# Kernel tuning notes

Measured on AMD Instinct MI355X. Metric: run time of the kernel, lower is better.

The kernel has to match this reference:

```python
import jax, jax.numpy as jnp
import numpy as np

N_ATOMS = 5000
N_EDGES = 100000
F = 128          # num_features
B = 20           # num_basis (sinc expansion)
L = 3            # num_interactions
CUTOFF = 5.0
NUM_EMB = 119


def setup_inputs() -> dict:
    key = jax.random.key(0)
    ks = jax.random.split(key, 16)
    Z = jax.random.randint(ks[0], (N_ATOMS,), 1, NUM_EMB)
    edge_idx = jax.random.randint(ks[1], (N_EDGES, 2), 0, N_ATOMS)
    edge_dist = jax.random.uniform(ks[2], (N_EDGES,), minval=0.5, maxval=6.0, dtype=jnp.float32)
    u = jax.random.normal(ks[3], (N_EDGES, 3), dtype=jnp.float32)
    u = u / jnp.linalg.norm(u, axis=-1, keepdims=True)
    edge_diff = u * edge_dist[:, None]  # displacement vectors with |d| == edge_dist
    s = lambda k, shape: (jax.random.normal(k, shape, dtype=jnp.float32) * 0.05)
    inp = dict(Z=Z, edge_idx=edge_idx, edge_diff=edge_diff, edge_dist=edge_dist)
    inp.update(
        emb=s(ks[4], (NUM_EMB, F)),
        msg_w1=s(ks[5], (L, F, F)), msg_b1=jnp.zeros((L, F), jnp.float32),
        msg_w2=s(ks[6], (L, F, 3 * F)), msg_b2=jnp.zeros((L, 3 * F), jnp.float32),
        filt_w=s(ks[7], (L, B, 3 * F)), filt_b=jnp.zeros((L, 3 * F), jnp.float32),
        upd_U=s(ks[8], (L, F, F)), upd_V=s(ks[9], (L, F, F)),
        upd_w1=s(ks[10], (L, 2 * F, F)), upd_b1=jnp.zeros((L, F), jnp.float32),
        upd_w2=s(ks[11], (L, F, 3 * F)), upd_b2=jnp.zeros((L, 3 * F), jnp.float32),
        ro_w1=s(ks[12], (F, F // 2)), ro_b1=jnp.zeros((F // 2,), jnp.float32),
        ro_w2=s(ks[13], (F // 2, 1)), ro_b2=jnp.zeros((1,), jnp.float32),
    )
    return inp


def _painn(Z, edge_idx, edge_diff, edge_dist,
           emb, msg_w1, msg_b1, msg_w2, msg_b2, filt_w, filt_b,
           upd_U, upd_V, upd_w1, upd_b1, upd_w2, upd_b2,
           ro_w1, ro_b1, ro_w2, ro_b2):
    dtype = edge_diff.dtype
    # edge mask (equivalent to boolean compaction: masked edges contribute 0)
    mask = (edge_dist < CUTOFF).astype(dtype)
    dst = edge_idx[:, 0]  # receiver (index_add target)
    src = edge_idx[:, 1]  # sender (gathered neighbor)
    # sinc radial expansion: sin(n*pi*r/rc)/r, n = 1..B
    n = jnp.arange(1, B + 1, dtype=dtype)
    rbf = jnp.sin(edge_dist[:, None] * n * (jnp.pi / CUTOFF)) / edge_dist[:, None]  # [E,B]
    # cosine cutoff envelope, zeroed outside cutoff
    fc = 0.5 * (jnp.cos(jnp.pi * edge_dist / CUTOFF) + 1.0)
    env = (fc * mask)[:, None]  # [E,1]
    unit = edge_diff / edge_dist[:, None]  # [E,3]

    s_feat = emb[Z]                                   # [N,F]
    v_feat = jnp.zeros((Z.shape[0], 3, F), dtype)     # [N,3,F]

    for l in range(L):
        # ---- PainnMessage ----
        filt = (rbf @ filt_w[l] + filt_b[l]) * env                           # [E,3F]
        phi = jax.nn.silu(s_feat @ msg_w1[l] + msg_b1[l]) @ msg_w2[l] + msg_b2[l]  # [N,3F]
        fo = filt * phi[src]                                                  # [E,3F]
        gsv, gev, ms = jnp.split(fo, 3, axis=-1)                              # each [E,F]
        mv = v_feat[src] * gsv[:, None, :] + gev[:, None, :] * unit[:, :, None]  # [E,3,F]
        s_feat = s_feat + jnp.zeros_like(s_feat).at[dst].add(ms)
        v_feat = v_feat + jnp.zeros_like(v_feat).at[dst].add(mv)
        # ---- PainnUpdate ----
        Uv = jnp.einsum('nif,fg->nig', v_feat, upd_U[l])   # [N,3,F]
        Vv = jnp.einsum('nif,fg->nig', v_feat, upd_V[l])   # [N,3,F]
        Vn = jnp.linalg.norm(Vv, axis=1)                   # [N,F]
        a = jax.nn.silu(jnp.concatenate([s_feat, Vn], axis=-1) @ upd_w1[l] + upd_b1[l]) @ upd_w2[l] + upd_b2[l]
        avv, asv, ass = jnp.split(a, 3, axis=-1)
        v_feat = v_feat + avv[:, None, :] * Uv
        s_feat = s_feat + asv * jnp.sum(Uv * Vv, axis=1) + ass

    # atomwise readout MLP -> per-atom energy
    atom_energy = (jax.nn.silu(s_feat @ ro_w1 + ro_b1) @ ro_w2 + ro_b2)[:, 0]  # [N]
    return atom_energy


def reference(Z, edge_idx, edge_diff, edge_dist,
              emb, msg_w1, msg_b1, msg_w2, msg_b2, filt_w, filt_b,
              upd_U, upd_V, upd_w1, upd_b1, upd_w2, upd_b2,
              ro_w1, ro_b1, ro_w2, ro_b2):
    return _painn(Z, edge_idx, edge_diff, edge_dist,
                  emb, msg_w1, msg_b1, msg_w2, msg_b2, filt_w, filt_b,
                  upd_U, upd_V, upd_w1, upd_b1, upd_w2, upd_b2,
                  ro_w1, ro_b1, ro_w2, ro_b2)
```

## Files before the change

kernel.cpp:

```cpp
#include <hip/hip_runtime.h>
#include <hip/hip_bf16.h>
#include <hip/hip_fp16.h>
#include <math.h>

#define N_ATOMS 5000
#define N_EDGES 100000
#define F 128
#define B 20
#define NL 3
#define CAP 64

constexpr float CUTOFF = 5.0f;
constexpr float PI_F = 3.14159265358979323846f;

typedef _Float16 f16x8 __attribute__((ext_vector_type(8)));
typedef _Float16 h2 __attribute__((ext_vector_type(2)));
typedef float f32x4 __attribute__((ext_vector_type(4)));

struct EMeta { int src; float env; float u0, u1, u2; int pad[3]; };

__device__ __forceinline__ float silu_f(float x) { return x / (1.0f + __expf(-x)); }

#define PV_IDX(atom, t) (((size_t)(atom) * F + (t)) * 8)

__global__ void init_kernel(const int* __restrict__ Z, const float* __restrict__ emb,
                            float* __restrict__ s, _Float16* __restrict__ s_h,
                            float* __restrict__ v, _Float16* __restrict__ pv,
                            int* __restrict__ count) {
    int atom = blockIdx.x;
    int t = threadIdx.x;
    float val = emb[Z[atom] * F + t];
    s[atom * F + t] = val;
    s_h[atom * F + t] = (_Float16)val;
#pragma unroll
    for (int d = 0; d < 3; ++d) v[(size_t)atom * 3 * F + d * F + t] = 0.0f;
    f16x8 z = {};
    *(f16x8*)(pv + PV_IDX(atom, t)) = z;
    if (t == 0) count[atom] = 0;
}

__global__ void fill_buckets(const int* __restrict__ eidx, int* __restrict__ count,
                             int* __restrict__ bucket) {
    int e = blockIdx.x * 256 + threadIdx.x;
    if (e >= N_EDGES) return;
    int dst = eidx[2 * e];
    int pos = atomicAdd(&count[dst], 1);
    if (pos < CAP) bucket[dst * CAP + pos] = e;
}

__global__ void edge_meta_kernel(const int* __restrict__ count, const int* __restrict__ bucket,
                                 const int* __restrict__ eidx, const float* __restrict__ ediff,
                                 const float* __restrict__ edist,
                                 EMeta* __restrict__ meta, _Float16* __restrict__ rbfh) {
    int slot = blockIdx.x * 256 + threadIdx.x;
    if (slot >= N_ATOMS * CAP) return;
    int a = slot / CAP, i = slot % CAP;
    if (i >= count[a]) return;
    int e = bucket[slot];
    float d = edist[e];
    EMeta m;
    m.src = eidx[2 * e + 1];
    float fc = 0.5f * (cosf(PI_F * d / CUTOFF) + 1.0f);
    m.env = (d < CUTOFF) ? fc : 0.0f;
    float inv = 1.0f / d;
    m.u0 = ediff[3 * e + 0] * inv;
    m.u1 = ediff[3 * e + 1] * inv;
    m.u2 = ediff[3 * e + 2] * inv;
    m.pad[0] = m.pad[1] = m.pad[2] = 0;
    meta[slot] = m;
    _Float16* rp = rbfh + (size_t)slot * 24;
#pragma unroll
    for (int b = 0; b < B; ++b)
        rp[b] = (_Float16)(sinf(d * (float)(b + 1) * (PI_F / CUTOFF)) / d);
    rp[20] = rp[21] = rp[22] = rp[23] = (_Float16)0.0f;
}

struct TPlanX { const float* src; void* dst; int R, C, blk0, isf16, pad; };
struct TPlansX { TPlanX p[24]; int n; };

__global__ void transpose_x(TPlansX P) {
    int b = blockIdx.x;
    int pi = 0;
#pragma unroll
    for (int i = 1; i < 24; ++i)
        if (i < P.n && b >= P.p[i].blk0) pi = i;
    const float* src = P.p[pi].src;
    int R = P.p[pi].R, C = P.p[pi].C, pad = P.p[pi].pad;
    int f = (b - P.p[pi].blk0) * 256 + threadIdx.x;
    if (f < R * C) {
        int c = f / R, r = f - c * R;
        float val = src[r * C + c];
        if (P.p[pi].isf16) ((_Float16*)P.p[pi].dst)[c * pad + r] = (_Float16)val;
        else ((float*)P.p[pi].dst)[c * pad + r] = val;
    }
}

__global__ __launch_bounds__(256) void phi_mlp_kernel(
    const _Float16* __restrict__ s_h, const _Float16* __restrict__ w1T,
    const float* __restrict__ b1, const _Float16* __restrict__ w2T,
    const float* __restrict__ b2, _Float16* __restrict__ pv) {
    __shared__ __align__(16) _Float16 shA[16 * 136];
    __shared__ __align__(16) _Float16 shH[16 * 136];
    int r0 = blockIdx.x * 16;
    int tid = threadIdx.x;
    {
        int r = tid >> 4, c8 = (tid & 15) * 8;
        int rg = r0 + r; if (rg >= N_ATOMS) rg = N_ATOMS - 1;
        *(f16x8*)(shA + r * 136 + c8) = *(const f16x8*)(s_h + (size_t)rg * F + c8);
    }
    __syncthreads();
    int lane = tid & 63, wv = tid >> 6;
    int col = lane & 15, quad = lane >> 4;
    for (int nt = wv; nt < 8; nt += 4) {
        int n = nt * 16 + col;
        f32x4 acc = {0.f, 0.f, 0.f, 0.f};
#pragma unroll
        for (int kt = 0; kt < 4; ++kt) {
            f16x8 afr = *(const f16x8*)(shA + col * 136 + kt * 32 + quad * 8);
            f16x8 bfr = *(const f16x8*)(w1T + (size_t)n * 128 + kt * 32 + quad * 8);
            acc = __builtin_amdgcn_mfma_f32_16x16x32_f16(afr, bfr, acc, 0, 0, 0);
        }
        float bb = b1[n];
#pragma unroll
        for (int r = 0; r < 4; ++r)
            shH[(quad * 4 + r) * 136 + n] = (_Float16)silu_f(acc[r] + bb);
    }
    __syncthreads();
    for (int nt = wv; nt < 24; nt += 4) {
        int n = nt * 16 + col;
        f32x4 acc = {0.f, 0.f, 0.f, 0.f};
#pragma unroll
        for (int kt = 0; kt < 4; ++kt) {
            f16x8 afr = *(const f16x8*)(shH + col * 136 + kt * 32 + quad * 8);
            f16x8 bfr = *(const f16x8*)(w2T + (size_t)n * 128 + kt * 32 + quad * 8);
            acc = __builtin_amdgcn_mfma_f32_16x16x32_f16(afr, bfr, acc, 0, 0, 0);
        }
        float bb = b2[n];
#pragma unroll
        for (int r = 0; r < 4; ++r) {
            int row = r0 + quad * 4 + r;
            if (row < N_ATOMS)
                pv[PV_IDX(row, n & 127) + (n >> 7)] = (_Float16)(acc[r] + bb);
        }
    }
}

__global__ __launch_bounds__(256) void edge_agg_kernel(
    const int* __restrict__ count, const EMeta* __restrict__ meta,
    const _Float16* __restrict__ rbfh,
    const _Float16* __restrict__ fwT,
    const float* __restrict__ fb,
    const _Float16* __restrict__ pv,
    float* __restrict__ s, float* __restrict__ v,
    _Float16* __restrict__ vmid_h) {
    int a = blockIdx.x;
    int tid = threadIdx.x;
    int t = tid & 127;
    int team = tid >> 7;

    unsigned int rw0[10], rw1[10], rw2[10];
    {
        const unsigned int* p0 = (const unsigned int*)(fwT + (size_t)t * 24);
        const unsigned int* p1 = (const unsigned int*)(fwT + (size_t)(F + t) * 24);
        const unsigned int* p2 = (const unsigned int*)(fwT + (size_t)(2 * F + t) * 24);
#pragma unroll
        for (int j = 0; j < 10; ++j) { rw0[j] = p0[j]; rw1[j] = p1[j]; rw2[j] = p2[j]; }
    }
    float fb0 = fb[t], fb1 = fb[F + t], fb2 = fb[2 * F + t];

    int n = count[a]; if (n > CAP) n = CAP;
    float accS = 0.f, accV0 = 0.f, accV1 = 0.f, accV2 = 0.f;

    __shared__ int sh_src[32];
    __shared__ float sh_env[32];
    __shared__ float sh_unit[32][3];
    __shared__ __align__(16) unsigned int sh_rbf[32 * 12];
    __shared__ __align__(16) float sh_part[4][F];
    const size_t aC = (size_t)a * CAP;
    const unsigned int* rbf32 = (const unsigned int*)rbfh;

    for (int base = 0; base < n; base += 32) {
        int cnt = min(32, n - base);
        __syncthreads();
        if (tid < cnt) {
            EMeta m = meta[aC + base + tid];
            sh_src[tid] = m.src;
            sh_env[tid] = m.env;
            sh_unit[tid][0] = m.u0; sh_unit[tid][1] = m.u1; sh_unit[tid][2] = m.u2;
        }
        for (int task = tid; task < cnt * 12; task += 256) {
            int i = task / 12, w = task - i * 12;
            sh_rbf[i * 12 + w] = rbf32[(aC + base + i) * 12 + w];
        }
        __syncthreads();

        int myCnt = (cnt > team) ? ((cnt - team + 1) >> 1) : 0;
        if (myCnt > 0) {
            f16x8 QA[4], QB[4];
            int ngrp = (myCnt + 3) >> 2;

            auto load_grp = [&](int gbase, f16x8 Q[4]) {
#pragma unroll
                for (int j = 0; j < 4; ++j) {
                    int i = gbase + j;
                    int ii = (i < myCnt) ? i : (myCnt - 1);
                    int src = sh_src[team + 2 * ii];
                    Q[j] = *(const f16x8*)(pv + PV_IDX(src, t));
                }
            };
            auto comp_grp = [&](int gbase, f16x8 Q[4]) {
#pragma unroll
                for (int j = 0; j < 4; ++j) {
                    int i = gbase + j;
                    if (i < myCnt) {
                        int ei = team + 2 * i;
                        const uint4* rq = (const uint4*)(sh_rbf + ei * 12);
                        uint4 qa = rq[0], qb = rq[1];
                        uint2 qc = *(const uint2*)(sh_rbf + ei * 12 + 8);
                        unsigned int rr[10] = {qa.x, qa.y, qa.z, qa.w,
                                               qb.x, qb.y, qb.z, qb.w, qc.x, qc.y};
                        float f0 = fb0, f1 = fb1, f2 = fb2;
#pragma unroll
                        for (int p = 0; p < 10; ++p) {
                            h2 rb = __builtin_bit_cast(h2, rr[p]);
                            f0 = __builtin_amdgcn_fdot2(rb, __builtin_bit_cast(h2, rw0[p]), f0, false);
                            f1 = __builtin_amdgcn_fdot2(rb, __builtin_bit_cast(h2, rw1[p]), f1, false);
                            f2 = __builtin_amdgcn_fdot2(rb, __builtin_bit_cast(h2, rw2[p]), f2, false);
                        }
                        float env = sh_env[ei];
                        f0 *= env; f1 *= env; f2 *= env;
                        accS += f2 * (float)Q[j][2];
                        float gsv = f0 * (float)Q[j][0];
                        float gev = f1 * (float)Q[j][1];
                        accV0 += (float)Q[j][3] * gsv + gev * sh_unit[ei][0];
                        accV1 += (float)Q[j][4] * gsv + gev * sh_unit[ei][1];
                        accV2 += (float)Q[j][5] * gsv + gev * sh_unit[ei][2];
                    }
                }
            };

            load_grp(0, QA);
            for (int g = 0; g < ngrp; g += 2) {
                if (g + 1 < ngrp) load_grp((g + 1) * 4, QB);
                comp_grp(g * 4, QA);
                if (g + 1 < ngrp) {
                    if (g + 2 < ngrp) load_grp((g + 2) * 4, QA);
                    comp_grp((g + 1) * 4, QB);
                }
            }
        }
    }

    __syncthreads();
    if (team == 1) {
        sh_part[0][t] = accS; sh_part[1][t] = accV0;
        sh_part[2][t] = accV1; sh_part[3][t] = accV2;
    }
    __syncthreads();
    if (team == 0) {
        float sm = s[a * F + t] + accS + sh_part[0][t];
        s[a * F + t] = sm;
        float vm0 = v[a * 3 * F + t] + accV0 + sh_part[1][t];
        float vm1 = v[a * 3 * F + F + t] + accV1 + sh_part[2][t];
        float vm2 = v[a * 3 * F + 2 * F + t] + accV2 + sh_part[3][t];
        v[a * 3 * F + t] = vm0;
        v[a * 3 * F + F + t] = vm1;
        v[a * 3 * F + 2 * F + t] = vm2;
        vmid_h[(size_t)(a * 3 + 0) * F + t] = (_Float16)vm0;
        vmid_h[(size_t)(a * 3 + 1) * F + t] = (_Float16)vm1;
        vmid_h[(size_t)(a * 3 + 2) * F + t] = (_Float16)vm2;
    }
}

__global__ __launch_bounds__(512) void fused_update_kernel(
    const _Float16* __restrict__ vmid_h, const _Float16* __restrict__ uvT,
    const _Float16* __restrict__ w1T, const float* __restrict__ b1,
    const _Float16* __restrict__ w2T, const float* __restrict__ b2,
    float* __restrict__ s, float* __restrict__ v, _Float16* __restrict__ pv,
    const _Float16* __restrict__ nw1T, const float* __restrict__ nb1,
    const _Float16* __restrict__ nw2T, const float* __restrict__ nb2,
    int do_phi,
    const _Float16* __restrict__ roT16, const float* __restrict__ rb1,
    const float* __restrict__ rw2, const float* __restrict__ rb2,
    float* __restrict__ out, int do_ro) {
    __shared__ __align__(16) _Float16 shA[48 * 136];
    __shared__ __align__(16) _Float16 shUV[48 * 264];
    __shared__ __align__(16) _Float16 shCat[16 * 264];
    __shared__ __align__(16) _Float16 shH[16 * 136];
    __shared__ __align__(16) _Float16 shAa[16 * 392];
    _Float16* shS = shA;
    float* shRO = (float*)shAa;
    int a0 = blockIdx.x * 16;
    int r0 = a0 * 3;
    int tid = threadIdx.x;
    for (int slot = tid; slot < 48 * 16; slot += 512) {
        int r = slot >> 4, c8 = (slot & 15) * 8;
        int rg = r0 + r; if (rg >= N_ATOMS * 3) rg = N_ATOMS * 3 - 1;
        *(f16x8*)(shA + r * 136 + c8) = *(const f16x8*)(vmid_h + (size_t)rg * F + c8);
    }
    __syncthreads();
    int lane = tid & 63, wv = tid >> 6;
    int col = lane & 15, quad = lane >> 4;

    for (int j = wv; j < 48; j += 8) {
        int mt = j >> 4, nt = j & 15;
        int n = nt * 16 + col;
        f32x4 acc = {0.f, 0.f, 0.f, 0.f};
#pragma unroll
        for (int kt = 0; kt < 4; ++kt) {
            f16x8 afr = *(const f16x8*)(shA + (mt * 16 + col) * 136 + kt * 32 + quad * 8);
            f16x8 bfr = *(const f16x8*)(uvT + (size_t)n * 128 + kt * 32 + quad * 8);
            acc = __builtin_amdgcn_mfma_f32_16x16x32_f16(afr, bfr, acc, 0, 0, 0);
        }
#pragma unroll
        for (int r = 0; r < 4; ++r)
            shUV[(mt * 16 + quad * 4 + r) * 264 + n] = (_Float16)acc[r];
    }
    __syncthreads();

    for (int p = tid; p < 2048; p += 512) {
        int ai = p >> 7, t = p & 127;
        int atom = a0 + ai;
        int ag = (atom < N_ATOMS) ? atom : N_ATOMS - 1;
        shCat[ai * 264 + t] = (_Float16)s[(size_t)ag * F + t];
        float x0 = (float)shUV[(ai * 3 + 0) * 264 + 128 + t];
        float x1 = (float)shUV[(ai * 3 + 1) * 264 + 128 + t];
        float x2 = (float)shUV[(ai * 3 + 2) * 264 + 128 + t];
        shCat[ai * 264 + 128 + t] = (_Float16)sqrtf(x0 * x0 + x1 * x1 + x2 * x2);
    }
    __syncthreads();

    for (int nt = wv; nt < 8; nt += 8) {
        int n = nt * 16 + col;
        f32x4 acc = {0.f, 0.f, 0.f, 0.f};
#pragma unroll
        for (int kt = 0; kt < 8; ++kt) {
            f16x8 afr = *(const f16x8*)(shCat + col * 264 + kt * 32 + quad * 8);
            f16x8 bfr = *(const f16x8*)(w1T + (size_t)n * 256 + kt * 32 + quad * 8);
            acc = __builtin_amdgcn_mfma_f32_16x16x32_f16(afr, bfr, acc, 0, 0, 0);
        }
        float bb = b1[n];
#pragma unroll
        for (int r = 0; r < 4; ++r)
            shH[(quad * 4 + r) * 136 + n] = (_Float16)silu_f(acc[r] + bb);
    }
    __syncthreads();

    for (int nt = wv; nt < 24; nt += 8) {
        int n = nt * 16 + col;
        f32x4 acc = {0.f, 0.f, 0.f, 0.f};
#pragma unroll
        for (int kt = 0; kt < 4; ++kt) {
            f16x8 afr = *(const f16x8*)(shH + col * 136 + kt * 32 + quad * 8);
            f16x8 bfr = *(const f16x8*)(w2T + (size_t)n * 128 + kt * 32 + quad * 8);
            acc = __builtin_amdgcn_mfma_f32_16x16x32_f16(afr, bfr, acc, 0, 0, 0);
        }
        float bb = b2[n];
#pragma unroll
        for (int r = 0; r < 4; ++r)
            shAa[(quad * 4 + r) * 392 + n] = (_Float16)(acc[r] + bb);
    }
    __syncthreads();

    for (int p = tid; p < 2048; p += 512) {
        int ai = p >> 7, t = p & 127;
        int atom = a0 + ai;
        if (atom >= N_ATOMS) { shS[ai * 136 + t] = (_Float16)0.0f; continue; }
        float avv = (float)shAa[ai * 392 + t];
        float asv = (float)shAa[ai * 392 + 128 + t];
        float ass = (float)shAa[ai * 392 + 256 + t];
        float dot = 0.f;
        _Float16* pvp = pv + PV_IDX(atom, t);
#pragma unroll
        for (int d = 0; d < 3; ++d) {
            float u = (float)shUV[(ai * 3 + d) * 264 + t];
            float w = (float)shUV[(ai * 3 + d) * 264 + 128 + t];
            dot += u * w;
            float nv = v[(size_t)atom * 3 * F + d * F + t] + avv * u;
            v[(size_t)atom * 3 * F + d * F + t] = nv;
            pvp[3 + d] = (_Float16)nv;
        }
        float sn = s[(size_t)atom * F + t] + asv * dot + ass;
        s[(size_t)atom * F + t] = sn;
        shS[ai * 136 + t] = (_Float16)sn;
    }

    if (do_phi) {
        __syncthreads();
        for (int nt = wv; nt < 8; nt += 8) {
            int n = nt * 16 + col;
            f32x4 acc = {0.f, 0.f, 0.f, 0.f};
#pragma unroll
            for (int kt = 0; kt < 4; ++kt) {
                f16x8 afr = *(const f16x8*)(shS + col * 136 + kt * 32 + quad * 8);
                f16x8 bfr = *(const f16x8*)(nw1T + (size_t)n * 128 + kt * 32 + quad * 8);
                acc = __builtin_amdgcn_mfma_f32_16x16x32_f16(afr, bfr, acc, 0, 0, 0);
            }
            float bb = nb1[n];
#pragma unroll
            for (int r = 0; r < 4; ++r)
                shH[(quad * 4 + r) * 136 + n] = (_Float16)silu_f(acc[r] + bb);
        }
        __syncthreads();
        for (int nt = wv; nt < 24; nt += 8) {
            int n = nt * 16 + col;
            f32x4 acc = {0.f, 0.f, 0.f, 0.f};
#pragma unroll
            for (int kt = 0; kt < 4; ++kt) {
                f16x8 afr = *(const f16x8*)(shH + col * 136 + kt * 32 + quad * 8);
                f16x8 bfr = *(const f16x8*)(nw2T + (size_t)n * 128 + kt * 32 + quad * 8);
                acc = __builtin_amdgcn_mfma_f32_16x16x32_f16(afr, bfr, acc, 0, 0, 0);
            }
            float bb = nb2[n];
#pragma unroll
            for (int r = 0; r < 4; ++r) {
                int row = a0 + quad * 4 + r;
                if (row < N_ATOMS)
                    pv[PV_IDX(row, n & 127) + (n >> 7)] = (_Float16)(acc[r] + bb);
            }
        }
    }

    if (do_ro) {
        __syncthreads();
        if (wv < 4) {
            int n = wv * 16 + col;
            f32x4 acc = {0.f, 0.f, 0.f, 0.f};
#pragma unroll
            for (int kt = 0; kt < 4; ++kt) {
                f16x8 afr = *(const f16x8*)(shS + col * 136 + kt * 32 + quad * 8);
                f16x8 bfr = *(const f16x8*)(roT16 + (size_t)n * 128 + kt * 32 + quad * 8);
                acc = __builtin_amdgcn_mfma_f32_16x16x32_f16(afr, bfr, acc, 0, 0, 0);
            }
            float bb = rb1[n], w2n = rw2[n];
#pragma unroll
            for (int r = 0; r < 4; ++r)
                shRO[(quad * 4 + r) * 68 + n] = silu_f(acc[r] + bb) * w2n;
        }
        __syncthreads();
        if (tid < 16) {
            int atom = a0 + tid;
            if (atom < N_ATOMS) {
                float sum = rb2[0];
#pragma unroll 8
                for (int k = 0; k < 64; ++k) sum += shRO[tid * 68 + k];
                out[atom] = sum;
            }
        }
    }
}

extern "C" void kernel_launch(void* const* d_in, const int* in_sizes, int n_in,
                              void* d_out, int out_size, void* d_ws, size_t ws_size,
                              hipStream_t stream) {
    const int*   Z      = (const int*)d_in[0];
    const int*   eidx   = (const int*)d_in[1];
    const float* ediff  = (const float*)d_in[2];
    const float* edist  = (const float*)d_in[3];
    const float* emb    = (const float*)d_in[4];
    const float* msg_w1 = (const float*)d_in[5];
    const float* msg_b1 = (const float*)d_in[6];
    const float* msg_w2 = (const float*)d_in[7];
    const float* msg_b2 = (const float*)d_in[8];
    const float* filt_w = (const float*)d_in[9];
    const float* filt_b = (const float*)d_in[10];
    const float* upd_U  = (const float*)d_in[11];
    const float* upd_V  = (const float*)d_in[12];
    const float* upd_w1 = (const float*)d_in[13];
    const float* upd_b1 = (const float*)d_in[14];
    const float* upd_w2 = (const float*)d_in[15];
    const float* upd_b2 = (const float*)d_in[16];
    const float* ro_w1  = (const float*)d_in[17];
    const float* ro_b1  = (const float*)d_in[18];
    const float* ro_w2  = (const float*)d_in[19];
    const float* ro_b2  = (const float*)d_in[20];
    float* out = (float*)d_out;

    float* ws = (float*)d_ws;
    float* s   = ws;
    float* v   = s + N_ATOMS * F;
    int* count  = (int*)(v + N_ATOMS * 3 * F);
    int* bucket = count + N_ATOMS;
    EMeta* meta = (EMeta*)(bucket + N_ATOMS * CAP);
    _Float16* rbfh = (_Float16*)(meta + N_ATOMS * CAP);
    _Float16* s_h    = rbfh + (size_t)N_ATOMS * CAP * 24;
    _Float16* vmid_h = s_h + (size_t)N_ATOMS * F;
    _Float16* pv     = vmid_h + (size_t)N_ATOMS * 3 * F;
    _Float16* wh     = pv + (size_t)N_ATOMS * F * 8;

    const int HWL = 16384 + 49152 + 32768 + 32768 + 49152 + 384 * 24;
    _Float16* mw1T = wh;
    _Float16* mw2T = wh + 16384;
    _Float16* uvT  = wh + 65536;
    _Float16* uw1T = wh + 98304;
    _Float16* uw2T = wh + 131072;
    _Float16* fwTl = wh + 180224;
    _Float16* roT16 = wh + (size_t)NL * HWL;

    TPlansX P; int nb = 0, pi = 0;
    auto add = [&](const float* src, void* dst, int R, int C, int isf16, int pad) {
        P.p[pi].src = src; P.p[pi].dst = dst; P.p[pi].R = R; P.p[pi].C = C;
        P.p[pi].blk0 = nb; P.p[pi].isf16 = isf16; P.p[pi].pad = pad;
        nb += (R * C + 255) / 256; ++pi;
    };
    for (int l = 0; l < NL; ++l) {
        add(msg_w1 + l * F * F,     mw1T + (size_t)l * HWL, F, F, 1, F);
        add(msg_w2 + l * F * 3 * F, mw2T + (size_t)l * HWL, F, 3 * F, 1, F);
        add(upd_U  + l * F * F,     uvT  + (size_t)l * HWL, F, F, 1, F);
        add(upd_V  + l * F * F,     uvT  + (size_t)l * HWL + F * F, F, F, 1, F);
        add(upd_w1 + l * 2 * F * F, uw1T + (size_t)l * HWL, 2 * F, F, 1, 2 * F);
        add(upd_w2 + l * F * 3 * F, uw2T + (size_t)l * HWL, F, 3 * F, 1, F);
        add(filt_w + l * B * 3 * F, fwTl + (size_t)l * HWL, B, 3 * F, 1, 24);
    }
    add(ro_w1, roT16, F, 64, 1, F);
    P.n = pi;

    init_kernel<<<N_ATOMS, F, 0, stream>>>(Z, emb, s, s_h, v, pv, count);
    fill_buckets<<<(N_EDGES + 255) / 256, 256, 0, stream>>>(eidx, count, bucket);
    transpose_x<<<nb, 256, 0, stream>>>(P);
    edge_meta_kernel<<<(N_ATOMS * CAP + 255) / 256, 256, 0, stream>>>(
        count, bucket, eidx, ediff, edist, meta, rbfh);

    const int GB16 = (N_ATOMS + 15) / 16;
    phi_mlp_kernel<<<GB16, 256, 0, stream>>>(
        s_h, mw1T, msg_b1, mw2T, msg_b2, pv);
    for (int l = 0; l < NL; ++l) {
        edge_agg_kernel<<<N_ATOMS, 256, 0, stream>>>(
            count, meta, rbfh, fwTl + (size_t)l * HWL, filt_b + l * 3 * F,
            pv, s, v, vmid_h);
        int do_phi = (l + 1 < NL);
        int do_ro = (l == NL - 1);
        int ln = do_phi ? (l + 1) : l;
        fused_update_kernel<<<GB16, 512, 0, stream>>>(
            vmid_h, uvT + (size_t)l * HWL,
            uw1T + (size_t)l * HWL, upd_b1 + l * F,
            uw2T + (size_t)l * HWL, upd_b2 + l * 3 * F,
            s, v, pv,
            mw1T + (size_t)ln * HWL, msg_b1 + ln * F,
            mw2T + (size_t)ln * HWL, msg_b2 + ln * 3 * F, do_phi,
            roT16, ro_b1, ro_w2, ro_b2, out, do_ro);
    }
}
```

Before: 366.8 us.

## Shrink packed per-atom message record to 6 halves and use 4 edge teams

The per-atom packed message record drops from 8 fp16 slots to 6, removing padding so each gathered neighbor read is 12 bytes instead of 16. The edge aggregation kernel also grows from 256 to 512 threads, splitting each atom's edges across four teams instead of two and reducing their partial sums through shared memory. The goal is less gather bandwidth and more latency hiding per atom. The cost is unaligned 12-byte loads that may split into several instructions, more shared-memory reduction, and larger blocks that could lower occupancy.

```diff
diff --git a/kernel.cpp b/kernel.cpp
--- a/kernel.cpp
+++ b/kernel.cpp
@@ -18,10 +18,11 @@
 typedef float f32x4 __attribute__((ext_vector_type(4)));
 
 struct EMeta { int src; float env; float u0, u1, u2; int pad[3]; };
+struct __align__(4) U3 { unsigned int x, y, z; };
 
 __device__ __forceinline__ float silu_f(float x) { return x / (1.0f + __expf(-x)); }
 
-#define PV_IDX(atom, t) (((size_t)(atom) * F + (t)) * 8)
+#define PV_IDX(atom, t) (((size_t)(atom) * F + (t)) * 6)
 
 __global__ void init_kernel(const int* __restrict__ Z, const float* __restrict__ emb,
                             float* __restrict__ s, _Float16* __restrict__ s_h,
@@ -34,8 +35,8 @@
     s_h[atom * F + t] = (_Float16)val;
 #pragma unroll
     for (int d = 0; d < 3; ++d) v[(size_t)atom * 3 * F + d * F + t] = 0.0f;
-    f16x8 z = {};
-    *(f16x8*)(pv + PV_IDX(atom, t)) = z;
+    unsigned int* pp = (unsigned int*)(pv + PV_IDX(atom, t));
+    pp[0] = 0u; pp[1] = 0u; pp[2] = 0u;
     if (t == 0) count[atom] = 0;
 }
 
@@ -145,7 +146,7 @@
     }
 }
 
-__global__ __launch_bounds__(256) void edge_agg_kernel(
+__global__ __launch_bounds__(512) void edge_agg_kernel(
     const int* __restrict__ count, const EMeta* __restrict__ meta,
     const _Float16* __restrict__ rbfh,
     const _Float16* __restrict__ fwT,
@@ -175,7 +176,7 @@
     __shared__ float sh_env[32];
     __shared__ float sh_unit[32][3];
     __shared__ __align__(16) unsigned int sh_rbf[32 * 12];
-    __shared__ __align__(16) float sh_part[4][F];
+    __shared__ __align__(16) float sh_part[3][4][F];
     const size_t aC = (size_t)a * CAP;
     const unsigned int* rbf32 = (const unsigned int*)rbfh;
 
@@ -188,32 +189,32 @@
             sh_env[tid] = m.env;
             sh_unit[tid][0] = m.u0; sh_unit[tid][1] = m.u1; sh_unit[tid][2] = m.u2;
         }
-        for (int task = tid; task < cnt * 12; task += 256) {
+        for (int task = tid; task < cnt * 12; task += 512) {
             int i = task / 12, w = task - i * 12;
             sh_rbf[i * 12 + w] = rbf32[(aC + base + i) * 12 + w];
         }
         __syncthreads();
 
-        int myCnt = (cnt > team) ? ((cnt - team + 1) >> 1) : 0;
+        int myCnt = (cnt > team) ? ((cnt - team + 3) >> 2) : 0;
         if (myCnt > 0) {
-            f16x8 QA[4], QB[4];
+            U3 QA[4], QB[4];
             int ngrp = (myCnt + 3) >> 2;
 
-            auto load_grp = [&](int gbase, f16x8 Q[4]) {
+            auto load_grp = [&](int gbase, U3 Q[4]) {
 #pragma unroll
                 for (int j = 0; j < 4; ++j) {
                     int i = gbase + j;
                     int ii = (i < myCnt) ? i : (myCnt - 1);
-                    int src = sh_src[team + 2 * ii];
-                    Q[j] = *(const f16x8*)(pv + PV_IDX(src, t));
+                    int src = sh_src[team + 4 * ii];
+                    Q[j] = *(const U3*)(pv + PV_IDX(src, t));
                 }
             };
-            auto comp_grp = [&](int gbase, f16x8 Q[4]) {
+            auto comp_grp = [&](int gbase, U3 Q[4]) {
 #pragma unroll
                 for (int j = 0; j < 4; ++j) {
                     int i = gbase + j;
                     if (i < myCnt) {
-                        int ei = team + 2 * i;
+                        int ei = team + 4 * i;
                         const uint4* rq = (const uint4*)(sh_rbf + ei * 12);
                         uint4 qa = rq[0], qb = rq[1];
                         uint2 qc = *(const uint2*)(sh_rbf + ei * 12 + 8);
@@ -229,12 +230,15 @@
                         }
                         float env = sh_env[ei];
                         f0 *= env; f1 *= env; f2 *= env;
-                        accS += f2 * (float)Q[j][2];
-                        float gsv = f0 * (float)Q[j][0];
-                        float gev = f1 * (float)Q[j][1];
-                        accV0 += (float)Q[j][3] * gsv + gev * sh_unit[ei][0];
-                        accV1 += (float)Q[j][4] * gsv + gev * sh_unit[ei][1];
-                        accV2 += (float)Q[j][5] * gsv + gev * sh_unit[ei][2];
+                        h2 q0 = __builtin_bit_cast(h2, Q[j].x);
+                        h2 q1 = __builtin_bit_cast(h2, Q[j].y);
+                        h2 q2 = __builtin_bit_cast(h2, Q[j].z);
+                        accS += f2 * (float)q1[0];
+                        float gsv = f0 * (float)q0[0];
+                        float gev = f1 * (float)q0[1];
+                        accV0 += (float)q1[1] * gsv + gev * sh_unit[ei][0];
+                        accV1 += (float)q2[0] * gsv + gev * sh_unit[ei][1];
+                        accV2 += (float)q2[1] * gsv + gev * sh_unit[ei][2];
                     }
                 }
             };
@@ -252,17 +256,17 @@
     }
 
     __syncthreads();
-    if (team == 1) {
-        sh_part[0][t] = accS; sh_part[1][t] = accV0;
-        sh_part[2][t] = accV1; sh_part[3][t] = accV2;
+    if (team >= 1) {
+        sh_part[team - 1][0][t] = accS; sh_part[team - 1][1][t] = accV0;
+        sh_part[team - 1][2][t] = accV1; sh_part[team - 1][3][t] = accV2;
     }
     __syncthreads();
     if (team == 0) {
-        float sm = s[a * F + t] + accS + sh_part[0][t];
+        float sm = s[a * F + t] + accS + sh_part[0][0][t] + sh_part[1][0][t] + sh_part[2][0][t];
         s[a * F + t] = sm;
-        float vm0 = v[a * 3 * F + t] + accV0 + sh_part[1][t];
-        float vm1 = v[a * 3 * F + F + t] + accV1 + sh_part[2][t];
-        float vm2 = v[a * 3 * F + 2 * F + t] + accV2 + sh_part[3][t];
+        float vm0 = v[a * 3 * F + t] + accV0 + sh_part[0][1][t] + sh_part[1][1][t] + sh_part[2][1][t];
+        float vm1 = v[a * 3 * F + F + t] + accV1 + sh_part[0][2][t] + sh_part[1][2][t] + sh_part[2][2][t];
+        float vm2 = v[a * 3 * F + 2 * F + t] + accV2 + sh_part[0][3][t] + sh_part[1][3][t] + sh_part[2][3][t];
         v[a * 3 * F + t] = vm0;
         v[a * 3 * F + F + t] = vm1;
         v[a * 3 * F + 2 * F + t] = vm2;
@@ -486,7 +490,7 @@
     _Float16* s_h    = rbfh + (size_t)N_ATOMS * CAP * 24;
     _Float16* vmid_h = s_h + (size_t)N_ATOMS * F;
     _Float16* pv     = vmid_h + (size_t)N_ATOMS * 3 * F;
-    _Float16* wh     = pv + (size_t)N_ATOMS * F * 8;
+    _Float16* wh     = pv + (size_t)N_ATOMS * F * 6;
 
     const int HWL = 16384 + 49152 + 32768 + 32768 + 49152 + 384 * 24;
     _Float16* mw1T = wh;
@@ -525,7 +529,7 @@
     phi_mlp_kernel<<<GB16, 256, 0, stream>>>(
         s_h, mw1T, msg_b1, mw2T, msg_b2, pv);
     for (int l = 0; l < NL; ++l) {
-        edge_agg_kernel<<<N_ATOMS, 256, 0, stream>>>(
+        edge_agg_kernel<<<N_ATOMS, 512, 0, stream>>>(
             count, meta, rbfh, fwTl + (size_t)l * HWL, filt_b + l * 3 * F,
             pv, s, v, vmid_h);
         int do_phi = (l + 1 < NL);
```

Result: slower. 398.2 us (+8.6%).
